# Kernel optimization log

Measured on AMD Instinct MI355X. Metric: run time of the kernel, lower is better.

Reference implementation:

```python
import jax, jax.numpy as jnp
import numpy as np

# Dimensions matching init_kwargs
O = 4096   # out_features
I = 4096   # in_features
R = 32     # svd_rank
G = 64     # n_groups
GS = I // G  # group_size = 64
NBITS = 4
NUM_BYTES = O * I * NBITS // 8


def setup_inputs() -> dict:
    key = jax.random.key(0)
    ks = jax.random.split(key, 7)
    return {
        "x": jax.random.normal(ks[0], (1, 4096, I), dtype=jnp.float32),
        # bit-packed int4 weights, two nibbles per byte (stored as int32 holding 0..255)
        "w_packed": jax.random.randint(ks[1], (NUM_BYTES,), 0, 256, dtype=jnp.int32),
        "svd_up": jax.random.normal(ks[2], (O, R), dtype=jnp.float32) * 0.02,
        "svd_down": jax.random.normal(ks[3], (R, I), dtype=jnp.float32) * 0.02,
        "scale": jax.random.uniform(ks[4], (O, G, 1), dtype=jnp.float32, minval=0.001, maxval=0.02),
        "zero_point": jax.random.uniform(ks[5], (O, G, 1), dtype=jnp.float32, minval=0.0, maxval=15.0),
        "bias": jax.random.normal(ks[6], (O,), dtype=jnp.float32) * 0.01,
    }


def _dequantize(w_packed, svd_up, svd_down, scale, zero_point):
    # Unpack two 4-bit values per byte (low nibble first).
    low = w_packed & 0xF
    high = (w_packed >> 4) & 0xF
    w_q = jnp.stack([low, high], axis=-1).reshape(O, G, GS).astype(jnp.float32)
    # Per-group affine dequant: (q - zero) * scale, then SVD low-rank correction.
    W = ((w_q - zero_point) * scale).reshape(O, I)
    return W + svd_up @ svd_down  # [O, I]


def reference(x, w_packed, svd_up, svd_down, scale, zero_point, bias):
    # forward_int8 path (tokens > 16, int8_matmul=True)
    W_f = _dequantize(w_packed, svd_up, svd_down, scale, zero_point).T  # [I, O]
    xm = x.reshape(-1, I)  # [N, I]
    # Dynamic per-row activation quant
    scale_x = jnp.max(jnp.abs(xm), axis=1, keepdims=True) / 127.0  # [N, 1]
    x_q = jnp.clip(jnp.round(xm / scale_x), -128, 127).astype(jnp.int8)
    # Dynamic per-column weight quant
    scale_w = jnp.max(jnp.abs(W_f), axis=0, keepdims=True) / 127.0  # [1, O]
    W_q = jnp.clip(jnp.round(W_f / scale_w), -128, 127).astype(jnp.int8)
    # int8 GEMM with int32 accumulation, then dequant scales + bias
    acc = jnp.matmul(x_q.astype(jnp.int32), W_q.astype(jnp.int32))  # [N, O] int32
    out = acc.astype(jnp.float32) * scale_x * scale_w + bias
    return out.reshape(*x.shape[:-1], O)
```

## Files before the change

### kernel.cpp

```cpp
#include <hip/hip_runtime.h>
#include <cstdint>
#include <cstddef>

#define I_DIM 4096
#define O_DIM 4096
#define RNK 32
#define NGRP 64
#define N_TOK 4096

typedef int v4i  __attribute__((ext_vector_type(4)));
typedef int v16i __attribute__((ext_vector_type(16)));

__device__ __forceinline__ int clamp_i8(float v) {
    int q = (int)rintf(v);
    q = q < -128 ? -128 : q;
    q = q > 127 ? 127 : q;
    return q;
}

#define BO 4
#define W_BLOCKS (O_DIM / BO)

__device__ __forceinline__ void quant_w_body(
    const int* __restrict__ w_packed, const float* __restrict__ svd_up,
    const float* __restrict__ svd_down, const float* __restrict__ scale,
    const float* __restrict__ zp, char* __restrict__ w_q,
    float* __restrict__ scale_w, int blk)
{
    __shared__ float s_sc[BO][NGRP];
    __shared__ float s_zp[BO][NGRP];
    __shared__ float s_red[BO][4];
    __shared__ float s_sw[BO];

    const int tid = threadIdx.x;
    const int o0 = blk * BO;

    for (int t = tid; t < BO * NGRP; t += 256) {
        s_sc[t >> 6][t & 63] = scale[(size_t)(o0 + (t >> 6)) * NGRP + (t & 63)];
        s_zp[t >> 6][t & 63] = zp[(size_t)(o0 + (t >> 6)) * NGRP + (t & 63)];
    }
    __syncthreads();

    float W[4][BO][4];

#pragma unroll
    for (int jq = 0; jq < 4; jq++) {
        const int q = tid + 256 * jq;
        const int g = q >> 4;
#pragma unroll
        for (int ro = 0; ro < BO; ro++) {
            const int2 b2 = *(const int2*)&w_packed[(size_t)(o0 + ro) * (I_DIM / 2) + 2 * q];
            const float sc = s_sc[ro][g], z = s_zp[ro][g];
            W[jq][ro][0] = ((float)(b2.x & 0xF) - z) * sc;
            W[jq][ro][1] = ((float)((b2.x >> 4) & 0xF) - z) * sc;
            W[jq][ro][2] = ((float)(b2.y & 0xF) - z) * sc;
            W[jq][ro][3] = ((float)((b2.y >> 4) & 0xF) - z) * sc;
        }
    }

#pragma unroll 2
    for (int r = 0; r < RNK; r++) {
        float u[BO];
#pragma unroll
        for (int ro = 0; ro < BO; ro++)
            u[ro] = svd_up[(size_t)(o0 + ro) * RNK + r];
        float4 d[4];
#pragma unroll
        for (int jq = 0; jq < 4; jq++)
            d[jq] = *(const float4*)&svd_down[(size_t)r * I_DIM + 4 * (tid + 256 * jq)];
#pragma unroll
        for (int jq = 0; jq < 4; jq++)
#pragma unroll
            for (int ro = 0; ro < BO; ro++) {
                W[jq][ro][0] += u[ro] * d[jq].x;
                W[jq][ro][1] += u[ro] * d[jq].y;
                W[jq][ro][2] += u[ro] * d[jq].z;
                W[jq][ro][3] += u[ro] * d[jq].w;
            }
    }

    float vmax[BO];
#pragma unroll
    for (int ro = 0; ro < BO; ro++) vmax[ro] = 0.0f;
#pragma unroll
    for (int jq = 0; jq < 4; jq++)
#pragma unroll
        for (int ro = 0; ro < BO; ro++)
            vmax[ro] = fmaxf(vmax[ro],
                fmaxf(fmaxf(fabsf(W[jq][ro][0]), fabsf(W[jq][ro][1])),
                      fmaxf(fabsf(W[jq][ro][2]), fabsf(W[jq][ro][3]))));

    const int lane = tid & 63, wv = tid >> 6;
#pragma unroll
    for (int ro = 0; ro < BO; ro++) {
        float m = vmax[ro];
        for (int off = 32; off > 0; off >>= 1)
            m = fmaxf(m, __shfl_down(m, off, 64));
        if (lane == 0) s_red[ro][wv] = m;
    }
    __syncthreads();
    if (tid < BO) {
        const float m = fmaxf(fmaxf(s_red[tid][0], s_red[tid][1]),
                              fmaxf(s_red[tid][2], s_red[tid][3]));
        const float sw = m / 127.0f;
        scale_w[o0 + tid] = sw;
        s_sw[tid] = sw;
    }
    __syncthreads();

    float inv[BO];
#pragma unroll
    for (int ro = 0; ro < BO; ro++) inv[ro] = 1.0f / s_sw[ro];

#pragma unroll
    for (int jq = 0; jq < 4; jq++) {
        const int q = tid + 256 * jq;
#pragma unroll
        for (int ro = 0; ro < BO; ro++) {
            const int q0 = clamp_i8(W[jq][ro][0] * inv[ro]);
            const int q1 = clamp_i8(W[jq][ro][1] * inv[ro]);
            const int q2 = clamp_i8(W[jq][ro][2] * inv[ro]);
            const int q3 = clamp_i8(W[jq][ro][3] * inv[ro]);
            ((int*)w_q)[(size_t)(o0 + ro) * (I_DIM / 4) + q] =
                (q0 & 0xFF) | ((q1 & 0xFF) << 8) | ((q2 & 0xFF) << 16) | ((q3 & 0xFF) << 24);
        }
    }
}

__device__ __forceinline__ void quant_x_body(
    const float* __restrict__ x, char* __restrict__ x_q,
    float* __restrict__ scale_x, int n)
{
    const int tid = threadIdx.x;
    const float4* xr = (const float4*)(x + (size_t)n * I_DIM);
    float4 v[4];
    float m = 0.0f;
#pragma unroll
    for (int j = 0; j < 4; j++) {
        v[j] = xr[tid + 256 * j];
        m = fmaxf(m, fmaxf(fmaxf(fabsf(v[j].x), fabsf(v[j].y)),
                           fmaxf(fabsf(v[j].z), fabsf(v[j].w))));
    }
    __shared__ float s_red[4];
    __shared__ float s_sx;
    for (int off = 32; off > 0; off >>= 1)
        m = fmaxf(m, __shfl_down(m, off, 64));
    if ((tid & 63) == 0) s_red[tid >> 6] = m;
    __syncthreads();
    if (tid == 0) {
        const float mm = fmaxf(fmaxf(s_red[0], s_red[1]),
                               fmaxf(s_red[2], s_red[3]));
        const float sx = mm / 127.0f;
        scale_x[n] = sx;
        s_sx = sx;
    }
    __syncthreads();
    const float sx = s_sx;
    int* outw = (int*)(x_q + (size_t)n * I_DIM);
#pragma unroll
    for (int j = 0; j < 4; j++) {
        const int q0 = clamp_i8(v[j].x / sx);
        const int q1 = clamp_i8(v[j].y / sx);
        const int q2 = clamp_i8(v[j].z / sx);
        const int q3 = clamp_i8(v[j].w / sx);
        outw[tid + 256 * j] =
            (q0 & 0xFF) | ((q1 & 0xFF) << 8) | ((q2 & 0xFF) << 16) | ((q3 & 0xFF) << 24);
    }
}

__global__ __launch_bounds__(256, 4) void prep_kernel(
    const int* __restrict__ w_packed, const float* __restrict__ svd_up,
    const float* __restrict__ svd_down, const float* __restrict__ scale,
    const float* __restrict__ zp, char* __restrict__ w_q,
    float* __restrict__ scale_w,
    const float* __restrict__ x, char* __restrict__ x_q,
    float* __restrict__ scale_x)
{
    if (blockIdx.x < W_BLOCKS)
        quant_w_body(w_packed, svd_up, svd_down, scale, zp, w_q, scale_w, blockIdx.x);
    else
        quant_x_body(x, x_q, scale_x, blockIdx.x - W_BLOCKS);
}

#define TBM 256
#define TBN 256
#define TBK 64
#define NKT (I_DIM / TBK)

__device__ __forceinline__ void stage_tile(const char* __restrict__ src, int row0,
                                           int t, char* lds_mat, int tid)
{
#pragma unroll
    for (int uu = 0; uu < 8; uu++) {
        const int q = tid + uu * 512;
        const int row = q >> 4;
        const int slot = q & 15;
        const int g = (slot >> 1) ^ ((row >> 1) & 7);
        const int w = slot & 1;
        const char* gsrc = src + (size_t)(row0 + row) * I_DIM + t * TBK + g * 8 + w * 4;
        __builtin_amdgcn_global_load_lds(
            (const __attribute__((address_space(1))) unsigned int*)gsrc,
            (__attribute__((address_space(3))) unsigned int*)(lds_mat + q * 4),
            4, 0, 0);
    }
}

#define READ_FRAGS(AF, BF, BUF, P) do {                                     \
    char* Ac_ = (BUF);                                                      \
    char* Bc_ = (BUF) + 16384;                                              \
    const int G0_ = ((P) * 2 + h) * 2;                                      \
    _Pragma("unroll")                                                       \
    for (int mt = 0; mt < 4; mt++) {                                        \
        const int row = wm * 128 + mt * 32 + l31;                           \
        const int ss = (row >> 1) & 7;                                      \
        const int2 lo = *(const int2*)(Ac_ + row * TBK + ((G0_ ^ ss) * 8)); \
        const int2 hi = *(const int2*)(Ac_ + row * TBK + (((G0_ + 1) ^ ss) * 8)); \
        AF[mt][0] = lo.x; AF[mt][1] = lo.y;                                 \
        AF[mt][2] = hi.x; AF[mt][3] = hi.y;                                 \
    }                                                                       \
    _Pragma("unroll")                                                       \
    for (int nt = 0; nt < 2; nt++) {                                        \
        const int row = wn * 64 + nt * 32 + l31;                            \
        const int ss = (row >> 1) & 7;                                      \
        const int2 lo = *(const int2*)(Bc_ + row * TBK + ((G0_ ^ ss) * 8)); \
        const int2 hi = *(const int2*)(Bc_ + row * TBK + (((G0_ + 1) ^ ss) * 8)); \
        BF[nt][0] = lo.x; BF[nt][1] = lo.y;                                 \
        BF[nt][2] = hi.x; BF[nt][3] = hi.y;                                 \
    }                                                                       \
} while (0)

#define MFMA_CLUSTER(AF, BF) do {                                           \
    __builtin_amdgcn_s_setprio(1);                                          \
    _Pragma("unroll")                                                       \
    for (int mt = 0; mt < 4; mt++)                                          \
        _Pragma("unroll")                                                   \
        for (int nt = 0; nt < 2; nt++)                                      \
            acc[mt][nt] = __builtin_amdgcn_mfma_i32_32x32x32_i8(            \
                AF[mt], BF[nt], acc[mt][nt], 0, 0, 0);                      \
    __builtin_amdgcn_s_setprio(0);                                          \
} while (0)

__global__ __launch_bounds__(512, 2) void gemm_i8_kernel(
    const char* __restrict__ x_q, const char* __restrict__ w_q,
    const float* __restrict__ scale_x, const float* __restrict__ scale_w,
    const float* __restrict__ bias, float* __restrict__ out)
{
    __shared__ v4i smem4[3 * 2 * 1024];
    char* lds = (char*)smem4;

    const int tid = threadIdx.x;
    const int id = blockIdx.x;
    const int xcd = id & 7;
    const int s = id >> 3;
    const int bm0 = (s & 15) * TBM;
    const int bn0 = (xcd * 2 + (s >> 4)) * TBN;

    const int lane = tid & 63, wv = tid >> 6;
    const int wm = wv >> 2, wn = wv & 3;
    const int l31 = lane & 31, h = lane >> 5;

    v16i acc[4][2];
#pragma unroll
    for (int mt = 0; mt < 4; mt++)
#pragma unroll
        for (int nt = 0; nt < 2; nt++)
            acc[mt][nt] = (v16i)(0);

    v4i a0[4], b0[2], a1[4], b1[2];

    stage_tile(x_q, bm0, 0, lds + 0 * 16384, tid);
    stage_tile(w_q, bn0, 0, lds + 1 * 16384, tid);
    stage_tile(x_q, bm0, 1, lds + 2 * 16384, tid);
    stage_tile(w_q, bn0, 1, lds + 3 * 16384, tid);
    asm volatile("s_waitcnt vmcnt(16)" ::: "memory");
    asm volatile("s_barrier" ::: "memory");
    READ_FRAGS(a0, b0, lds + 0 * 32768, 0);

    int cb = 0, nb = 2;
    for (int t = 0; t < NKT; ++t) {
        char* bufc = lds + cb * 32768;
        const bool pf = (t + 2 < NKT);

        if (pf) stage_tile(x_q, bm0, t + 2, lds + nb * 32768, tid);
        READ_FRAGS(a1, b1, bufc, 1);
        MFMA_CLUSTER(a0, b0);
        if (pf) stage_tile(w_q, bn0, t + 2, lds + nb * 32768 + 16384, tid);

        if (t < NKT - 1) {
            if (t < NKT - 2) asm volatile("s_waitcnt vmcnt(16)" ::: "memory");
            else             asm volatile("s_waitcnt vmcnt(0)" ::: "memory");
            asm volatile("s_waitcnt lgkmcnt(0)" ::: "memory");
            asm volatile("s_barrier" ::: "memory");
            char* bufn = lds + ((cb == 2) ? 0 : cb + 1) * 32768;
            READ_FRAGS(a0, b0, bufn, 0);
        }
        MFMA_CLUSTER(a1, b1);

        cb = (cb == 2) ? 0 : cb + 1;
        nb = (nb == 2) ? 0 : nb + 1;
    }

#pragma unroll
    for (int mt = 0; mt < 4; mt++) {
        const int rbase = bm0 + wm * 128 + mt * 32 + 4 * h;
        float sx[16];
#pragma unroll
        for (int reg = 0; reg < 16; reg++)
            sx[reg] = scale_x[rbase + (reg & 3) + 8 * (reg >> 2)];
#pragma unroll
        for (int nt = 0; nt < 2; nt++) {
            const int oc = bn0 + wn * 64 + nt * 32 + l31;
            const float sw = scale_w[oc];
            const float bs = bias[oc];
#pragma unroll
            for (int reg = 0; reg < 16; reg++) {
                const int rr = rbase + (reg & 3) + 8 * (reg >> 2);
                out[(size_t)rr * O_DIM + oc] =
                    (float)acc[mt][nt][reg] * sx[reg] * sw + bs;
            }
        }
    }
}

extern "C" void kernel_launch(void* const* d_in, const int* in_sizes, int n_in,
                              void* d_out, int out_size, void* d_ws, size_t ws_size,
                              hipStream_t stream) {
    const float* x        = (const float*)d_in[0];
    const int*   w_packed = (const int*)d_in[1];
    const float* svd_up   = (const float*)d_in[2];
    const float* svd_down = (const float*)d_in[3];
    const float* scale    = (const float*)d_in[4];
    const float* zp       = (const float*)d_in[5];
    const float* bias     = (const float*)d_in[6];
    float* out = (float*)d_out;

    char* ws = (char*)d_ws;
    char*  w_q     = ws;
    char*  x_q     = ws + ((size_t)16 << 20);
    float* scale_w = (float*)(ws + ((size_t)32 << 20));
    float* scale_x = (float*)(ws + ((size_t)32 << 20) + 16384);

    prep_kernel<<<W_BLOCKS + N_TOK, 256, 0, stream>>>(
        w_packed, svd_up, svd_down, scale, zp, w_q, scale_w, x, x_q, scale_x);
    gemm_i8_kernel<<<(N_TOK / TBM) * (O_DIM / TBN), 512, 0, stream>>>(
        x_q, w_q, scale_x, scale_w, bias, out);
}
```

Measured before the change: 266.1 us.

## Stage GEMM tiles through registers with 16-byte loads instead of direct-to-LDS loads

Replaces the 4-byte global_load_lds staging with 16-byte vector global loads into registers, followed by swizzled ds_write into the triple-buffered LDS ring. A register double buffer keeps loads three k-tiles ahead, and the loop is unrolled by two so the buffers alternate. The goal is fewer, wider memory instructions and no vmcnt waits on direct LDS loads. In exchange it uses more VGPRs under the 512-thread, 2-block launch bound, and it relies on the compiler inserting vmcnt waits before the ds_writes.

```diff
diff --git a/kernel.cpp b/kernel.cpp
--- a/kernel.cpp
+++ b/kernel.cpp
@@ -186,24 +186,6 @@
 #define TBN 256
 #define TBK 64
 #define NKT (I_DIM / TBK)
-
-__device__ __forceinline__ void stage_tile(const char* __restrict__ src, int row0,
-                                           int t, char* lds_mat, int tid)
-{
-#pragma unroll
-    for (int uu = 0; uu < 8; uu++) {
-        const int q = tid + uu * 512;
-        const int row = q >> 4;
-        const int slot = q & 15;
-        const int g = (slot >> 1) ^ ((row >> 1) & 7);
-        const int w = slot & 1;
-        const char* gsrc = src + (size_t)(row0 + row) * I_DIM + t * TBK + g * 8 + w * 4;
-        __builtin_amdgcn_global_load_lds(
-            (const __attribute__((address_space(1))) unsigned int*)gsrc,
-            (__attribute__((address_space(3))) unsigned int*)(lds_mat + q * 4),
-            4, 0, 0);
-    }
-}
 
 #define READ_FRAGS(AF, BF, BUF, P) do {                                     \
     char* Ac_ = (BUF);                                                      \
@@ -240,6 +222,43 @@
     __builtin_amdgcn_s_setprio(0);                                          \
 } while (0)
 
+#define GLOAD(A0_, A1_, B0_, B1_, t) do {                                   \
+    A0_ = *(const v4i*)(gA0 + (size_t)(t) * TBK);                           \
+    A1_ = *(const v4i*)(gA1 + (size_t)(t) * TBK);                           \
+    B0_ = *(const v4i*)(gB0 + (size_t)(t) * TBK);                           \
+    B1_ = *(const v4i*)(gB1 + (size_t)(t) * TBK);                           \
+} while (0)
+
+#define DSWRITE(A0_, A1_, B0_, B1_, bufp) do {                              \
+    char* Ab_ = (bufp); char* Bb_ = (bufp) + 16384;                         \
+    int2 w_;                                                                \
+    w_.x = A0_[0]; w_.y = A0_[1]; *(int2*)(Ab_ + wo00) = w_;                \
+    w_.x = A0_[2]; w_.y = A0_[3]; *(int2*)(Ab_ + wo01) = w_;                \
+    w_.x = A1_[0]; w_.y = A1_[1]; *(int2*)(Ab_ + wo10) = w_;                \
+    w_.x = A1_[2]; w_.y = A1_[3]; *(int2*)(Ab_ + wo11) = w_;                \
+    w_.x = B0_[0]; w_.y = B0_[1]; *(int2*)(Bb_ + wo00) = w_;                \
+    w_.x = B0_[2]; w_.y = B0_[3]; *(int2*)(Bb_ + wo01) = w_;                \
+    w_.x = B1_[0]; w_.y = B1_[1]; *(int2*)(Bb_ + wo10) = w_;                \
+    w_.x = B1_[2]; w_.y = B1_[3]; *(int2*)(Bb_ + wo11) = w_;                \
+} while (0)
+
+#define BODY(t, CA0, CA1, CB0, CB1, NA0, NA1, NB0, NB1) do {                \
+    char* bufc = lds + cb * 32768;                                          \
+    if ((t) + 3 < NKT) GLOAD(NA0, NA1, NB0, NB1, (t) + 3);                  \
+    READ_FRAGS(a1, b1, bufc, 1);                                            \
+    MFMA_CLUSTER(a0, b0);                                                   \
+    if ((t) + 2 < NKT) DSWRITE(CA0, CA1, CB0, CB1, lds + nb * 32768);       \
+    if ((t) < NKT - 1) {                                                    \
+        asm volatile("s_waitcnt lgkmcnt(0)" ::: "memory");                  \
+        asm volatile("s_barrier" ::: "memory");                             \
+        char* bufn = lds + ((cb == 2) ? 0 : cb + 1) * 32768;                \
+        READ_FRAGS(a0, b0, bufn, 0);                                        \
+    }                                                                       \
+    MFMA_CLUSTER(a1, b1);                                                   \
+    cb = (cb == 2) ? 0 : cb + 1;                                            \
+    nb = (nb == 2) ? 0 : nb + 1;                                            \
+} while (0)
+
 __global__ __launch_bounds__(512, 2) void gemm_i8_kernel(
     const char* __restrict__ x_q, const char* __restrict__ w_q,
     const float* __restrict__ scale_x, const float* __restrict__ scale_w,
@@ -259,6 +278,18 @@
     const int wm = wv >> 2, wn = wv & 3;
     const int l31 = lane & 31, h = lane >> 5;
 
+    const int c0 = tid, c1 = tid + 512;
+    const int r0s = c0 >> 2, r1s = c1 >> 2;
+    const char* gA0 = x_q + (size_t)(bm0 + r0s) * I_DIM + (c0 & 3) * 16;
+    const char* gA1 = x_q + (size_t)(bm0 + r1s) * I_DIM + (c1 & 3) * 16;
+    const char* gB0 = w_q + (size_t)(bn0 + r0s) * I_DIM + (c0 & 3) * 16;
+    const char* gB1 = w_q + (size_t)(bn0 + r1s) * I_DIM + (c1 & 3) * 16;
+    const int s0s = (r0s >> 1) & 7, s1s = (r1s >> 1) & 7;
+    const int wo00 = r0s * TBK + ((2 * (c0 & 3)    ) ^ s0s) * 8;
+    const int wo01 = r0s * TBK + ((2 * (c0 & 3) + 1) ^ s0s) * 8;
+    const int wo10 = r1s * TBK + ((2 * (c1 & 3)    ) ^ s1s) * 8;
+    const int wo11 = r1s * TBK + ((2 * (c1 & 3) + 1) ^ s1s) * 8;
+
     v16i acc[4][2];
 #pragma unroll
     for (int mt = 0; mt < 4; mt++)
@@ -267,37 +298,22 @@
             acc[mt][nt] = (v16i)(0);
 
     v4i a0[4], b0[2], a1[4], b1[2];
-
-    stage_tile(x_q, bm0, 0, lds + 0 * 16384, tid);
-    stage_tile(w_q, bn0, 0, lds + 1 * 16384, tid);
-    stage_tile(x_q, bm0, 1, lds + 2 * 16384, tid);
-    stage_tile(w_q, bn0, 1, lds + 3 * 16384, tid);
-    asm volatile("s_waitcnt vmcnt(16)" ::: "memory");
+    v4i sA0, sA1, sB0, sB1;
+    v4i tA0, tA1, tB0, tB1;
+
+    GLOAD(sA0, sA1, sB0, sB1, 0);
+    GLOAD(tA0, tA1, tB0, tB1, 1);
+    DSWRITE(sA0, sA1, sB0, sB1, lds + 0 * 32768);
+    GLOAD(sA0, sA1, sB0, sB1, 2);
+    DSWRITE(tA0, tA1, tB0, tB1, lds + 1 * 32768);
+    asm volatile("s_waitcnt lgkmcnt(0)" ::: "memory");
     asm volatile("s_barrier" ::: "memory");
     READ_FRAGS(a0, b0, lds + 0 * 32768, 0);
 
     int cb = 0, nb = 2;
-    for (int t = 0; t < NKT; ++t) {
-        char* bufc = lds + cb * 32768;
-        const bool pf = (t + 2 < NKT);
-
-        if (pf) stage_tile(x_q, bm0, t + 2, lds + nb * 32768, tid);
-        READ_FRAGS(a1, b1, bufc, 1);
-        MFMA_CLUSTER(a0, b0);
-        if (pf) stage_tile(w_q, bn0, t + 2, lds + nb * 32768 + 16384, tid);
-
-        if (t < NKT - 1) {
-            if (t < NKT - 2) asm volatile("s_waitcnt vmcnt(16)" ::: "memory");
-            else             asm volatile("s_waitcnt vmcnt(0)" ::: "memory");
-            asm volatile("s_waitcnt lgkmcnt(0)" ::: "memory");
-            asm volatile("s_barrier" ::: "memory");
-            char* bufn = lds + ((cb == 2) ? 0 : cb + 1) * 32768;
-            READ_FRAGS(a0, b0, bufn, 0);
-        }
-        MFMA_CLUSTER(a1, b1);
-
-        cb = (cb == 2) ? 0 : cb + 1;
-        nb = (nb == 2) ? 0 : nb + 1;
+    for (int t = 0; t < NKT; t += 2) {
+        BODY(t,     sA0, sA1, sB0, sB1, tA0, tA1, tB0, tB1);
+        BODY(t + 1, tA0, tA1, tB0, tB1, sA0, sA1, sB0, sB1);
     }
 
 #pragma unroll
```

Result: faster. 258.8 us (-2.7%).
